# Performance work log

Measured on AMD Instinct MI355X. Metric: run time of the kernel, lower is better.

The kernel has to match this reference:

```python
import jax, jax.numpy as jnp
import numpy as np

B, S, D_IN, D_OUT, H = 4, 2048, 1024, 1024, 16
DH = D_OUT // H


def setup_inputs() -> dict:
    key = jax.random.key(0)
    k1, k2, k3 = jax.random.split(key, 3)
    payload = jax.random.normal(k1, (B, S, D_IN), dtype=jnp.float32)
    w_qkv = jax.random.normal(k2, (D_IN, 3 * D_OUT), dtype=jnp.float32) * (D_IN ** -0.5)
    w_out = jax.random.normal(k3, (D_OUT, D_OUT), dtype=jnp.float32) * (D_OUT ** -0.5)
    b_out = jnp.zeros((D_OUT,), dtype=jnp.float32)
    return {"payload": payload, "w_qkv": w_qkv, "w_out": w_out, "b_out": b_out}


def reference(payload, w_qkv, w_out, b_out):
    b, t, _ = payload.shape
    h, dh = H, DH
    qkv = payload @ w_qkv  # [b, t, 3*D_OUT]
    q, k, v = jnp.split(qkv, 3, axis=-1)
    # [b, t, h, dh] -> [b, h, t, dh]
    q = q.reshape(b, t, h, dh).transpose(0, 2, 1, 3)
    k = k.reshape(b, t, h, dh).transpose(0, 2, 1, 3)
    v = v.reshape(b, t, h, dh).transpose(0, 2, 1, 3)
    scores = jnp.einsum("bhqd,bhkd->bhqk", q, k) / jnp.sqrt(jnp.float32(dh))
    causal = jnp.tril(jnp.ones((t, t), dtype=bool))  # True = keep
    scores = jnp.where(causal, scores, -jnp.inf)
    weights = jax.nn.softmax(scores, axis=-1)
    # dropout_rate = 0.0 -> identity
    ctx = jnp.einsum("bhqk,bhkd->bhqd", weights, v)
    ctx = ctx.transpose(0, 2, 1, 3).reshape(b, t, h * dh)
    return ctx @ w_out + b_out
```

## Files before the change

kernel.cpp:

```cpp
#include <hip/hip_runtime.h>

#define NB 4
#define NS 2048
#define NH 16
#define NDH 64

typedef short bf16x8 __attribute__((ext_vector_type(8)));
typedef short bf16x4 __attribute__((ext_vector_type(4)));
typedef float f32x4 __attribute__((ext_vector_type(4)));
typedef unsigned short u16;
typedef unsigned int u32;

static __device__ __forceinline__ u16 f2bf(float f) {
  unsigned u = __float_as_uint(f);
  u += 0x7fffu + ((u >> 16) & 1u);
  return (u16)(u >> 16);
}

#define GLDS(gp, lp) __builtin_amdgcn_global_load_lds( \
    (const __attribute__((address_space(1))) void*)(gp), \
    (__attribute__((address_space(3))) void*)(lp), 16, 0, 0)

__global__ void cvt_k(const float* __restrict__ in, u16* __restrict__ out, int n) {
  int i = (blockIdx.x * 256 + threadIdx.x) * 8;
  if (i >= n) return;
  float4 a = *(const float4*)&in[i];
  float4 b = *(const float4*)&in[i + 4];
  bf16x8 u;
  u[0] = (short)f2bf(a.x); u[1] = (short)f2bf(a.y);
  u[2] = (short)f2bf(a.z); u[3] = (short)f2bf(a.w);
  u[4] = (short)f2bf(b.x); u[5] = (short)f2bf(b.y);
  u[6] = (short)f2bf(b.z); u[7] = (short)f2bf(b.w);
  *(bf16x8*)&out[i] = u;
}

__global__ void trcvt_k(const float* __restrict__ in, u16* __restrict__ out, int R, int C) {
  __shared__ float t[32][33];
  int c0 = blockIdx.x * 32, r0 = blockIdx.y * 32;
  int tx = threadIdx.x & 7, ty = threadIdx.x >> 3;
  float4 v = *(const float4*)&in[(size_t)(r0 + ty) * C + c0 + tx * 4];
  t[ty][tx * 4 + 0] = v.x; t[ty][tx * 4 + 1] = v.y;
  t[ty][tx * 4 + 2] = v.z; t[ty][tx * 4 + 3] = v.w;
  __syncthreads();
  ushort4 o;
  o.x = f2bf(t[tx * 4 + 0][ty]); o.y = f2bf(t[tx * 4 + 1][ty]);
  o.z = f2bf(t[tx * 4 + 2][ty]); o.w = f2bf(t[tx * 4 + 3][ty]);
  *(ushort4*)&out[(size_t)(c0 + ty) * R + r0 + tx * 4] = o;
}

template<int MODE, int WM>
__global__ __launch_bounds__(WM * 128)
void gemm_k(const u16* __restrict__ A, const u16* __restrict__ Bt,
            int M, int N, int K,
            u16* __restrict__ Qo, u16* __restrict__ Ko, u16* __restrict__ VTo,
            float* __restrict__ Co, const float* __restrict__ bias) {
  constexpr int T  = WM * 128;
  constexpr int BM = WM * 64;
  constexpr int RA = 4;
  constexpr int RB = 1024 / T;
  __shared__ __align__(16) u16 As[BM * 64];
  __shared__ __align__(16) u16 Bs[128 * 64];
  const int tid = threadIdx.x;
  const int w = tid >> 6, l = tid & 63;
  const int lr = l & 15, lg = l >> 4;
  const int wr = w >> 1, wc = w & 1;

  const int L = blockIdx.x + gridDim.x * blockIdx.y;
  const int xcd = L & 7, li = L >> 3;
  const int bx = li % gridDim.x;
  const int by = xcd * (gridDim.y >> 3) + li / gridDim.x;

  const int m0 = by * BM, n0 = bx * 128;
  const int swz = (lr & 7) << 4;

  f32x4 acc[4][4] = {};

  const int nk = K >> 6;
  for (int kt = 0; kt < nk; ++kt) {
    __syncthreads();
    const int k0 = kt * 64;
#pragma unroll
    for (int r2 = 0; r2 < RA; ++r2) {
      int c = r2 * T + tid;
      int row = c >> 3;
      int scolb = ((c & 7) * 16) ^ ((row & 7) << 4);
      GLDS(A + (size_t)(m0 + row) * K + k0 + (scolb >> 1),
           (char*)As + (size_t)r2 * T * 16 + w * 1024);
    }
#pragma unroll
    for (int r2 = 0; r2 < RB; ++r2) {
      int c = r2 * T + tid;
      int row = c >> 3;
      int scolb = ((c & 7) * 16) ^ ((row & 7) << 4);
      GLDS(Bt + (size_t)(n0 + row) * K + k0 + (scolb >> 1),
           (char*)Bs + (size_t)r2 * T * 16 + w * 1024);
    }
    __syncthreads();

#pragma unroll
    for (int kk = 0; kk < 2; ++kk) {
      bf16x8 af[4];
#pragma unroll
      for (int mi = 0; mi < 4; ++mi)
        af[mi] = *(const bf16x8*)((const char*)As +
                  ((wr * 64 + mi * 16 + lr) * 128 + ((kk * 64 + lg * 16) ^ swz)));
#pragma unroll
      for (int ni = 0; ni < 4; ++ni) {
        bf16x8 bfr = *(const bf16x8*)((const char*)Bs +
                  ((wc * 64 + ni * 16 + lr) * 128 + ((kk * 64 + lg * 16) ^ swz)));
#pragma unroll
        for (int mi = 0; mi < 4; ++mi)
          acc[mi][ni] = __builtin_amdgcn_mfma_f32_16x16x32_bf16(af[mi], bfr, acc[mi][ni], 0, 0, 0);
      }
    }
  }

#pragma unroll
  for (int mi = 0; mi < 4; ++mi) {
#pragma unroll
    for (int ni = 0; ni < 4; ++ni) {
#pragma unroll
      for (int r = 0; r < 4; ++r) {
        int gm = m0 + wr * 64 + mi * 16 + lg * 4 + r;
        int gn = n0 + wc * 64 + ni * 16 + lr;
        float v = acc[mi][ni][r];
        if (MODE == 0) {
          int which = gn >> 10, hd = gn & 1023;
          int b = gm >> 11, s = gm & 2047;
          int bh = b * NH + (hd >> 6), dh = hd & 63;
          if (which == 0)      Qo[((size_t)bh * NS + s) * NDH + dh] = f2bf(v * 0.1803368801111204f);
          else if (which == 1) Ko[((size_t)bh * NS + s) * NDH + dh] = f2bf(v);
          else                 VTo[((size_t)bh * NDH + dh) * NS + s] = f2bf(v);
        } else {
          Co[(size_t)gm * N + gn] = v + bias[gn];
        }
      }
    }
  }
}

__global__ __launch_bounds__(512)
void attn_k(const u16* __restrict__ Q, const u16* __restrict__ Kg,
            const u16* __restrict__ VTg, u16* __restrict__ CTX) {
  const int bh = blockIdx.x;
  const int pr = blockIdx.y;
  const int tid = threadIdx.x, w = tid >> 6, l = tid & 63;
  const int lr = l & 15, lg = l >> 4;
  const u16* Qh  = Q   + (size_t)bh * NS * NDH;
  const u16* Kh  = Kg  + (size_t)bh * NS * NDH;
  const u16* Vth = VTg + (size_t)bh * NDH * NS;

  __shared__ __align__(16) u16 Ks[2][64 * 64];
  __shared__ __align__(16) u16 Vs[2][64 * 64];

  const int srow_ = tid >> 3;
  const int colb  = (tid & 7) * 16;
  const int scolb = colb ^ ((srow_ & 7) << 4);
  const int kSrcOff = srow_ * NDH + (scolb >> 1);
  const int vSrcOff = srow_ * NS + (scolb >> 1);
  const int ldsOff  = w * 1024;

#define STAGE(t, buf) do {                                          \
    GLDS(Kh  + (size_t)(t) * 64 * NDH + kSrcOff, (char*)Ks[buf] + ldsOff); \
    GLDS(Vth + (size_t)(t) * 64       + vSrcOff, (char*)Vs[buf] + ldsOff); \
  } while (0)

  const int swz = (lr & 7) << 4;
  const int b = bh >> 4, h = bh & 15;

  for (int pass = 0; pass < 2; ++pass) {
    const int qt = pass == 0 ? pr : 15 - pr;

    const int qrow = qt * 128 + w * 16 + lr;
    bf16x8 qf[2];
    qf[0] = *(const bf16x8*)&Qh[(size_t)qrow * NDH + 0 * 32 + lg * 8];
    qf[1] = *(const bf16x8*)&Qh[(size_t)qrow * NDH + 1 * 32 + lg * 8];

    f32x4 o[4] = {};
    float lrun = 0.f;
    const int qmin = qt * 128 + w * 16;

    __syncthreads();
    STAGE(0, 0);
    __syncthreads();

    const int NT = 2 * qt + 2;
    for (int kt = 0; kt < NT; ++kt) {
      const int cur = kt & 1;
      if (kt + 1 < NT) STAGE(kt + 1, cur ^ 1);

      f32x4 sc[4] = {};
#pragma unroll
      for (int kk = 0; kk < 2; ++kk) {
#pragma unroll
        for (int kg = 0; kg < 4; ++kg) {
          bf16x8 kf = *(const bf16x8*)((const char*)Ks[cur] +
                       ((kg * 16 + lr) * 128 + ((kk * 64 + lg * 16) ^ swz)));
          sc[kg] = __builtin_amdgcn_mfma_f32_16x16x32_bf16(kf, qf[kk], sc[kg], 0, 0, 0);
        }
      }

      float sum = 0.f;
      if (kt * 64 + 63 > qmin) {
#pragma unroll
        for (int kg = 0; kg < 4; ++kg)
#pragma unroll
          for (int r = 0; r < 4; ++r) {
            int kglob = kt * 64 + kg * 16 + lg * 4 + r;
            float e = (kglob > qrow) ? 0.f : exp2f(sc[kg][r]);
            sc[kg][r] = e; sum += e;
          }
      } else {
#pragma unroll
        for (int kg = 0; kg < 4; ++kg)
#pragma unroll
          for (int r = 0; r < 4; ++r) {
            float e = exp2f(sc[kg][r]);
            sc[kg][r] = e; sum += e;
          }
      }
      lrun += sum;

#pragma unroll
      for (int half = 0; half < 2; ++half) {
        union { u32 wd[4]; bf16x8 v; } pk;
#pragma unroll
        for (int w2 = 0; w2 < 4; ++w2) {
          float lo = sc[half * 2 + (w2 >> 1)][2 * (w2 & 1)];
          float hi = sc[half * 2 + (w2 >> 1)][2 * (w2 & 1) + 1];
          asm("v_cvt_pk_bf16_f32 %0, %1, %2" : "=v"(pk.wd[w2]) : "v"(lo), "v"(hi));
        }
        bf16x8 pf = pk.v;
#pragma unroll
        for (int dhg = 0; dhg < 4; ++dhg) {
          const char* vrow = (const char*)Vs[cur] + (dhg * 16 + lr) * 128;
          bf16x4 va = *(const bf16x4*)(vrow + ((half * 64 + lg * 8) ^ swz));
          bf16x4 vb = *(const bf16x4*)(vrow + ((half * 64 + 32 + lg * 8) ^ swz));
          bf16x8 vf = __builtin_shufflevector(va, vb, 0, 1, 2, 3, 4, 5, 6, 7);
          o[dhg] = __builtin_amdgcn_mfma_f32_16x16x32_bf16(pf, vf, o[dhg], 0, 0, 0);
        }
      }

      __syncthreads();
    }

    lrun += __shfl_xor(lrun, 16);
    lrun += __shfl_xor(lrun, 32);
    float linv = 1.0f / lrun;
#pragma unroll
    for (int r = 0; r < 4; ++r) {
      float lq = __shfl(linv, (l & 48) | (lg * 4 + r));
      int srow = qt * 128 + w * 16 + lg * 4 + r;
      size_t base = ((size_t)(b * NS + srow)) * (NH * NDH) + h * NDH;
#pragma unroll
      for (int dhg = 0; dhg < 4; ++dhg)
        CTX[base + dhg * 16 + lr] = f2bf(o[dhg][r] * lq);
    }
  }
#undef STAGE
}

extern "C" void kernel_launch(void* const* d_in, const int* in_sizes, int n_in,
                              void* d_out, int out_size, void* d_ws, size_t ws_size,
                              hipStream_t stream) {
  const float* payload = (const float*)d_in[0];
  const float* w_qkv   = (const float*)d_in[1];
  const float* w_out   = (const float*)d_in[2];
  const float* b_out   = (const float*)d_in[3];
  float* out = (float*)d_out;

  char* ws = (char*)d_ws;
  size_t o0 = 0;
  u16* Xb    = (u16*)(ws + o0); o0 += (size_t)8192 * 1024 * 2;
  u16* Wqkvt = (u16*)(ws + o0); o0 += (size_t)3072 * 1024 * 2;
  u16* Woutt = (u16*)(ws + o0); o0 += (size_t)1024 * 1024 * 2;
  u16* Qb    = (u16*)(ws + o0); o0 += (size_t)64 * 2048 * 64 * 2;
  u16* Kb    = (u16*)(ws + o0); o0 += (size_t)64 * 2048 * 64 * 2;
  u16* VTb   = (u16*)(ws + o0); o0 += (size_t)64 * 64 * 2048 * 2;
  u16* CTX   = Xb;

  cvt_k<<<dim3(4096), dim3(256), 0, stream>>>(payload, Xb, 8192 * 1024);
  trcvt_k<<<dim3(96, 32), dim3(256), 0, stream>>>(w_qkv, Wqkvt, 1024, 3072);
  trcvt_k<<<dim3(32, 32), dim3(256), 0, stream>>>(w_out, Woutt, 1024, 1024);
  gemm_k<0, 4><<<dim3(24, 32), dim3(512), 0, stream>>>(Xb, Wqkvt, 8192, 3072, 1024,
                                                       Qb, Kb, VTb, nullptr, nullptr);
  attn_k<<<dim3(64, 8), dim3(512), 0, stream>>>(Qb, Kb, VTb, CTX);
  gemm_k<1, 2><<<dim3(8, 64), dim3(256), 0, stream>>>(CTX, Woutt, 8192, 1024, 1024,
                                                      nullptr, nullptr, nullptr, out, b_out);
}
```

Baseline: 193.6 us.

## Fuse conversion kernels into one launch and double attention KV tile size

Merges the three fp32-to-bf16 convert and transpose kernels into a single prep kernel dispatched by block index, removing two launches. In attention, each staged K/V tile grows from 64 to 128 keys, processed as two 64-key sub-blocks per barrier, which halves the number of __syncthreads and stage rounds. The cost is doubled LDS use per block (64 KB total), which may reduce occupancy, plus slightly more causal-mask work on the final tile, since the diagonal now falls inside a 128-key tile.

```diff
diff --git a/kernel.cpp b/kernel.cpp
--- a/kernel.cpp
+++ b/kernel.cpp
@@ -21,22 +21,33 @@
     (const __attribute__((address_space(1))) void*)(gp), \
     (__attribute__((address_space(3))) void*)(lp), 16, 0, 0)
 
-__global__ void cvt_k(const float* __restrict__ in, u16* __restrict__ out, int n) {
-  int i = (blockIdx.x * 256 + threadIdx.x) * 8;
-  if (i >= n) return;
-  float4 a = *(const float4*)&in[i];
-  float4 b = *(const float4*)&in[i + 4];
-  bf16x8 u;
-  u[0] = (short)f2bf(a.x); u[1] = (short)f2bf(a.y);
-  u[2] = (short)f2bf(a.z); u[3] = (short)f2bf(a.w);
-  u[4] = (short)f2bf(b.x); u[5] = (short)f2bf(b.y);
-  u[6] = (short)f2bf(b.z); u[7] = (short)f2bf(b.w);
-  *(bf16x8*)&out[i] = u;
-}
-
-__global__ void trcvt_k(const float* __restrict__ in, u16* __restrict__ out, int R, int C) {
+__global__ void prep_k(const float* __restrict__ payload, const float* __restrict__ w_qkv,
+                       const float* __restrict__ w_out, u16* __restrict__ Xb,
+                       u16* __restrict__ Wqkvt, u16* __restrict__ Woutt) {
   __shared__ float t[32][33];
-  int c0 = blockIdx.x * 32, r0 = blockIdx.y * 32;
+  const int bid = blockIdx.x;
+  if (bid < 4096) {
+    int i = (bid * 256 + threadIdx.x) * 8;
+    float4 a = *(const float4*)&payload[i];
+    float4 b = *(const float4*)&payload[i + 4];
+    bf16x8 u;
+    u[0] = (short)f2bf(a.x); u[1] = (short)f2bf(a.y);
+    u[2] = (short)f2bf(a.z); u[3] = (short)f2bf(a.w);
+    u[4] = (short)f2bf(b.x); u[5] = (short)f2bf(b.y);
+    u[6] = (short)f2bf(b.z); u[7] = (short)f2bf(b.w);
+    *(bf16x8*)&Xb[i] = u;
+    return;
+  }
+  const float* in;  u16* out;  int R, C, c0, r0;
+  if (bid < 4096 + 3072) {
+    int b2 = bid - 4096;
+    in = w_qkv; out = Wqkvt; R = 1024; C = 3072;
+    c0 = (b2 % 96) * 32; r0 = (b2 / 96) * 32;
+  } else {
+    int b3 = bid - 7168;
+    in = w_out; out = Woutt; R = 1024; C = 1024;
+    c0 = (b3 & 31) * 32; r0 = (b3 >> 5) * 32;
+  }
   int tx = threadIdx.x & 7, ty = threadIdx.x >> 3;
   float4 v = *(const float4*)&in[(size_t)(r0 + ty) * C + c0 + tx * 4];
   t[ty][tx * 4 + 0] = v.x; t[ty][tx * 4 + 1] = v.y;
@@ -150,19 +161,27 @@
   const u16* Kh  = Kg  + (size_t)bh * NS * NDH;
   const u16* Vth = VTg + (size_t)bh * NDH * NS;
 
-  __shared__ __align__(16) u16 Ks[2][64 * 64];
-  __shared__ __align__(16) u16 Vs[2][64 * 64];
-
-  const int srow_ = tid >> 3;
-  const int colb  = (tid & 7) * 16;
-  const int scolb = colb ^ ((srow_ & 7) << 4);
-  const int kSrcOff = srow_ * NDH + (scolb >> 1);
-  const int vSrcOff = srow_ * NS + (scolb >> 1);
-  const int ldsOff  = w * 1024;
-
-#define STAGE(t, buf) do {                                          \
-    GLDS(Kh  + (size_t)(t) * 64 * NDH + kSrcOff, (char*)Ks[buf] + ldsOff); \
-    GLDS(Vth + (size_t)(t) * 64       + vSrcOff, (char*)Vs[buf] + ldsOff); \
+  __shared__ __align__(16) u16 Ks[2][128 * 64];
+  __shared__ __align__(16) u16 Vs[2][64 * 128];
+
+  const int kRow0 = tid >> 3,         kColb = (tid & 7) * 16;
+  const int kRow1 = 64 + (tid >> 3);
+  const int vRow0 = tid >> 4,         vColb = (tid & 15) * 16;
+  const int vRow1 = 32 + (tid >> 4);
+  const int kSrc0 = kRow0 * NDH + ((kColb ^ ((kRow0 & 7) << 4)) >> 1);
+  const int kSrc1 = kRow1 * NDH + ((kColb ^ ((kRow1 & 7) << 4)) >> 1);
+  const int vSrc0 = vRow0 * NS + ((vColb ^ ((vRow0 & 7) << 4)) >> 1);
+  const int vSrc1 = vRow1 * NS + ((vColb ^ ((vRow1 & 7) << 4)) >> 1);
+  const int ldsOff0 = w * 1024;
+  const int ldsOff1 = 8192 + w * 1024;
+
+#define STAGE(t, buf) do {                                            \
+    const u16* Kt_ = Kh  + (size_t)(t) * 128 * NDH;                   \
+    const u16* Vt_ = Vth + (size_t)(t) * 128;                         \
+    GLDS(Kt_ + kSrc0, (char*)Ks[buf] + ldsOff0);                      \
+    GLDS(Kt_ + kSrc1, (char*)Ks[buf] + ldsOff1);                      \
+    GLDS(Vt_ + vSrc0, (char*)Vs[buf] + ldsOff0);                      \
+    GLDS(Vt_ + vSrc1, (char*)Vs[buf] + ldsOff1);                      \
   } while (0)
 
   const int swz = (lr & 7) << 4;
@@ -184,60 +203,64 @@
     STAGE(0, 0);
     __syncthreads();
 
-    const int NT = 2 * qt + 2;
+    const int NT = qt + 1;
     for (int kt = 0; kt < NT; ++kt) {
       const int cur = kt & 1;
       if (kt + 1 < NT) STAGE(kt + 1, cur ^ 1);
 
-      f32x4 sc[4] = {};
-#pragma unroll
-      for (int kk = 0; kk < 2; ++kk) {
-#pragma unroll
-        for (int kg = 0; kg < 4; ++kg) {
-          bf16x8 kf = *(const bf16x8*)((const char*)Ks[cur] +
-                       ((kg * 16 + lr) * 128 + ((kk * 64 + lg * 16) ^ swz)));
-          sc[kg] = __builtin_amdgcn_mfma_f32_16x16x32_bf16(kf, qf[kk], sc[kg], 0, 0, 0);
+#pragma unroll
+      for (int sub = 0; sub < 2; ++sub) {
+        f32x4 sc[4] = {};
+#pragma unroll
+        for (int kk = 0; kk < 2; ++kk) {
+#pragma unroll
+          for (int kg = 0; kg < 4; ++kg) {
+            bf16x8 kf = *(const bf16x8*)((const char*)Ks[cur] +
+                         ((sub * 64 + kg * 16 + lr) * 128 + ((kk * 64 + lg * 16) ^ swz)));
+            sc[kg] = __builtin_amdgcn_mfma_f32_16x16x32_bf16(kf, qf[kk], sc[kg], 0, 0, 0);
+          }
         }
-      }
-
-      float sum = 0.f;
-      if (kt * 64 + 63 > qmin) {
-#pragma unroll
-        for (int kg = 0; kg < 4; ++kg)
-#pragma unroll
-          for (int r = 0; r < 4; ++r) {
-            int kglob = kt * 64 + kg * 16 + lg * 4 + r;
-            float e = (kglob > qrow) ? 0.f : exp2f(sc[kg][r]);
-            sc[kg][r] = e; sum += e;
+
+        const int kbase = kt * 128 + sub * 64;
+        float sum = 0.f;
+        if (kbase + 63 > qmin) {
+#pragma unroll
+          for (int kg = 0; kg < 4; ++kg)
+#pragma unroll
+            for (int r = 0; r < 4; ++r) {
+              int kglob = kbase + kg * 16 + lg * 4 + r;
+              float e = (kglob > qrow) ? 0.f : exp2f(sc[kg][r]);
+              sc[kg][r] = e; sum += e;
+            }
+        } else {
+#pragma unroll
+          for (int kg = 0; kg < 4; ++kg)
+#pragma unroll
+            for (int r = 0; r < 4; ++r) {
+              float e = exp2f(sc[kg][r]);
+              sc[kg][r] = e; sum += e;
+            }
+        }
+        lrun += sum;
+
+#pragma unroll
+        for (int half = 0; half < 2; ++half) {
+          union { u32 wd[4]; bf16x8 v; } pk;
+#pragma unroll
+          for (int w2 = 0; w2 < 4; ++w2) {
+            float lo = sc[half * 2 + (w2 >> 1)][2 * (w2 & 1)];
+            float hi = sc[half * 2 + (w2 >> 1)][2 * (w2 & 1) + 1];
+            asm("v_cvt_pk_bf16_f32 %0, %1, %2" : "=v"(pk.wd[w2]) : "v"(lo), "v"(hi));
           }
-      } else {
-#pragma unroll
-        for (int kg = 0; kg < 4; ++kg)
-#pragma unroll
-          for (int r = 0; r < 4; ++r) {
-            float e = exp2f(sc[kg][r]);
-            sc[kg][r] = e; sum += e;
+          bf16x8 pf = pk.v;
+#pragma unroll
+          for (int dhg = 0; dhg < 4; ++dhg) {
+            const char* vrow = (const char*)Vs[cur] + (dhg * 16 + lr) * 256;
+            bf16x4 va = *(const bf16x4*)(vrow + sub * 128 + ((half * 64 + lg * 8) ^ swz));
+            bf16x4 vb = *(const bf16x4*)(vrow + sub * 128 + ((half * 64 + 32 + lg * 8) ^ swz));
+            bf16x8 vf = __builtin_shufflevector(va, vb, 0, 1, 2, 3, 4, 5, 6, 7);
+            o[dhg] = __builtin_amdgcn_mfma_f32_16x16x32_bf16(pf, vf, o[dhg], 0, 0, 0);
           }
-      }
-      lrun += sum;
-
-#pragma unroll
-      for (int half = 0; half < 2; ++half) {
-        union { u32 wd[4]; bf16x8 v; } pk;
-#pragma unroll
-        for (int w2 = 0; w2 < 4; ++w2) {
-          float lo = sc[half * 2 + (w2 >> 1)][2 * (w2 & 1)];
-          float hi = sc[half * 2 + (w2 >> 1)][2 * (w2 & 1) + 1];
-          asm("v_cvt_pk_bf16_f32 %0, %1, %2" : "=v"(pk.wd[w2]) : "v"(lo), "v"(hi));
-        }
-        bf16x8 pf = pk.v;
-#pragma unroll
-        for (int dhg = 0; dhg < 4; ++dhg) {
-          const char* vrow = (const char*)Vs[cur] + (dhg * 16 + lr) * 128;
-          bf16x4 va = *(const bf16x4*)(vrow + ((half * 64 + lg * 8) ^ swz));
-          bf16x4 vb = *(const bf16x4*)(vrow + ((half * 64 + 32 + lg * 8) ^ swz));
-          bf16x8 vf = __builtin_shufflevector(va, vb, 0, 1, 2, 3, 4, 5, 6, 7);
-          o[dhg] = __builtin_amdgcn_mfma_f32_16x16x32_bf16(pf, vf, o[dhg], 0, 0, 0);
         }
       }
 
@@ -279,9 +302,7 @@
   u16* VTb   = (u16*)(ws + o0); o0 += (size_t)64 * 64 * 2048 * 2;
   u16* CTX   = Xb;
 
-  cvt_k<<<dim3(4096), dim3(256), 0, stream>>>(payload, Xb, 8192 * 1024);
-  trcvt_k<<<dim3(96, 32), dim3(256), 0, stream>>>(w_qkv, Wqkvt, 1024, 3072);
-  trcvt_k<<<dim3(32, 32), dim3(256), 0, stream>>>(w_out, Woutt, 1024, 1024);
+  prep_k<<<dim3(8192), dim3(256), 0, stream>>>(payload, w_qkv, w_out, Xb, Wqkvt, Woutt);
   gemm_k<0, 4><<<dim3(24, 32), dim3(512), 0, stream>>>(Xb, Wqkvt, 8192, 3072, 1024,
                                                        Qb, Kb, VTb, nullptr, nullptr);
   attn_k<<<dim3(64, 8), dim3(512), 0, stream>>>(Qb, Kb, VTb, CTX);
```

Result: faster. 186.2 us (median of 4 runs) (-3.8%).
